# Kernel tuning notes

Hardware: AMD Instinct MI355X
Metric: run time of the kernel (lower is better)

Reference implementation:

```python
import jax, jax.numpy as jnp
import numpy as np

C = 512
IC = C // 2
BN_EPS = 1e-5

def conv1x1(x, w, b):
    # x: (b,c,h,w), w: (o,c), b: (o,)
    return jnp.einsum('bchw,oc->bohw', x, w) + b[None, :, None, None]

def setup_inputs() -> dict:
    key = jax.random.key(0)
    ks = jax.random.split(key, 9)
    b, h, w = 8, 48, 48
    x = jax.random.normal(ks[0], (b, C, h, w), dtype=jnp.float32)
    s = 1.0 / np.sqrt(C)
    g_w = jax.random.normal(ks[1], (IC, C), dtype=jnp.float32) * s
    g_b = jnp.zeros((IC,), jnp.float32)
    theta_w = jax.random.normal(ks[2], (IC, C), dtype=jnp.float32) * s
    theta_b = jnp.zeros((IC,), jnp.float32)
    phi_w = jax.random.normal(ks[3], (IC, C), dtype=jnp.float32) * s
    phi_b = jnp.zeros((IC,), jnp.float32)
    w_w = jax.random.normal(ks[4], (C, IC), dtype=jnp.float32) * (1.0 / np.sqrt(IC))
    w_b = jnp.zeros((C,), jnp.float32)
    # BatchNorm affine params: initialized to 0 per nn.init.constant_ in source
    bn_gamma = jnp.zeros((C,), jnp.float32)
    bn_beta = jnp.zeros((C,), jnp.float32)
    return {"x": x, "g_w": g_w, "g_b": g_b, "theta_w": theta_w, "theta_b": theta_b,
            "phi_w": phi_w, "phi_b": phi_b, "w_w": w_w, "w_b": w_b,
            "bn_gamma": bn_gamma, "bn_beta": bn_beta}

def reference(x, g_w, g_b, theta_w, theta_b, phi_w, phi_b, w_w, w_b, bn_gamma, bn_beta):
    b, c, h, w = x.shape
    hw = h * w
    g_x = conv1x1(x, g_w, g_b).reshape(b, IC, hw).transpose(0, 2, 1)      # (b,hw,ic)
    theta_x = conv1x1(x, theta_w, theta_b).reshape(b, IC, hw).transpose(0, 2, 1)  # (b,hw,ic)
    phi_x = conv1x1(x, phi_w, phi_b).reshape(b, IC, hw)                    # (b,ic,hw)
    f = jnp.einsum('bqc,bck->bqk', theta_x, phi_x)                         # (b,hw,hw), unscaled
    f_div_C = jax.nn.softmax(f, axis=-1)
    y = jnp.einsum('bqk,bkc->bqc', f_div_C, g_x)                           # (b,hw,ic)
    y = y.transpose(0, 2, 1).reshape(b, IC, h, w)
    wy = conv1x1(y, w_w, w_b)                                              # (b,c,h,w)
    # BatchNorm2d in training mode: batch statistics over (b,h,w)
    mean = jnp.mean(wy, axis=(0, 2, 3), keepdims=True)
    var = jnp.var(wy, axis=(0, 2, 3), keepdims=True)
    wy_bn = (wy - mean) / jnp.sqrt(var + BN_EPS)
    wy_bn = wy_bn * bn_gamma[None, :, None, None] + bn_beta[None, :, None, None]
    return wy_bn + x
```

## Files before the change

### kernel.cpp

```cpp
#include <hip/hip_runtime.h>
#include <hip/hip_bf16.h>
#include <stdint.h>

constexpr int Bn  = 8;
constexpr int Cc  = 512;
constexpr int ICc = 256;
constexpr int HWc = 48 * 48;
constexpr float BN_EPS = 1e-5f;

typedef unsigned short u16;
typedef __attribute__((ext_vector_type(8))) short short8;
typedef __attribute__((ext_vector_type(4))) float f32x4;

__device__ __forceinline__ u16 f2bf(float f) {
    uint32_t u = __builtin_bit_cast(uint32_t, f);
    u += 0x7fffu + ((u >> 16) & 1u);
    return (u16)(u >> 16);
}
__device__ __forceinline__ float bf2f(u16 h) {
    uint32_t u = ((uint32_t)h) << 16;
    return __builtin_bit_cast(float, u);
}
__device__ __forceinline__ void load_lds16(const void* g, void* l) {
    __builtin_amdgcn_global_load_lds(
        (const __attribute__((address_space(1))) void*)(uintptr_t)g,
        (__attribute__((address_space(3))) void*)(uintptr_t)l, 16, 0, 0);
}
template <int N> __device__ __forceinline__ void wait_vmcnt() {
    if constexpr (N == 0)      asm volatile("s_waitcnt vmcnt(0)" ::: "memory");
    else if constexpr (N == 3) asm volatile("s_waitcnt vmcnt(3)" ::: "memory");
    else if constexpr (N == 4) asm volatile("s_waitcnt vmcnt(4)" ::: "memory");
    else if constexpr (N == 6) asm volatile("s_waitcnt vmcnt(6)" ::: "memory");
    else if constexpr (N == 8) asm volatile("s_waitcnt vmcnt(8)" ::: "memory");
}
__device__ __forceinline__ void wait_lgkm0() {
    asm volatile("s_waitcnt lgkmcnt(0)" ::: "memory");
}
__device__ __forceinline__ void barrier_fenced() {
    __builtin_amdgcn_s_barrier();
    asm volatile("" ::: "memory");
}

__global__ __launch_bounds__(256)
void cast_front(const float* __restrict__ th_w, const float* __restrict__ ph_w,
                const float* __restrict__ g_w, const float* __restrict__ th_b,
                const float* __restrict__ ph_b, u16* __restrict__ wcat,
                float* __restrict__ bias_thph) {
    int idx = blockIdx.x * 256 + threadIdx.x;
    if (idx < 98304) {
        const float4* src;
        if (idx < 32768)       src = (const float4*)th_w + idx;
        else if (idx < 65536)  src = (const float4*)ph_w + (idx - 32768);
        else                   src = (const float4*)g_w  + (idx - 65536);
        float4 v = *src;
        ushort4 o;
        o.x = f2bf(v.x); o.y = f2bf(v.y); o.z = f2bf(v.z); o.w = f2bf(v.w);
        ((ushort4*)wcat)[idx] = o;
    } else if (idx < 98816) {
        int i = idx - 98304;
        bias_thph[i] = (i < 256) ? th_b[i] : ph_b[i - 256];
    }
}

__global__ __launch_bounds__(256)
void cast_w(const float* __restrict__ a, u16* __restrict__ out) {
    int idx = blockIdx.x * 256 + threadIdx.x;
    float4 v = ((const float4*)a)[idx];
    ushort4 o;
    o.x = f2bf(v.x); o.y = f2bf(v.y); o.z = f2bf(v.z); o.w = f2bf(v.w);
    ((ushort4*)out)[idx] = o;
}

__global__ __launch_bounds__(256)
void transpose_cast_x(const float* __restrict__ x, u16* __restrict__ xt) {
    __shared__ float t[64][33];
    const int b = blockIdx.z;
    const int p0 = blockIdx.x * 32;
    const int c0 = blockIdx.y * 64;
    const int tx = threadIdx.x & 31, ty = threadIdx.x >> 5;
    const float* xb = x + (size_t)b * Cc * HWc;
#pragma unroll
    for (int r = 0; r < 8; ++r)
        t[r * 8 + ty][tx] = xb[(size_t)(c0 + r * 8 + ty) * HWc + p0 + tx];
    __syncthreads();
    u16* xtb = xt + (size_t)b * HWc * Cc;
    const int cc = (threadIdx.x & 31) * 2, pp = threadIdx.x >> 5;
#pragma unroll
    for (int r = 0; r < 4; ++r) {
        int p = r * 8 + pp;
        ushort2 v;
        v.x = f2bf(t[cc][p]);
        v.y = f2bf(t[cc + 1][p]);
        *(ushort2*)&xtb[(size_t)(p0 + p) * Cc + c0 + cc] = v;
    }
}

template <int TM, int STORE, bool STATS>
__global__ __launch_bounds__(256, 2)
void mfma_gemm(const u16* __restrict__ A, const u16* __restrict__ B,
               void* __restrict__ Cout, const float* __restrict__ bias,
               int bias_mode, int K, int ldA, int ldB, int ldC,
               size_t sA, size_t sB, size_t sC,
               float* __restrict__ s0g, float* __restrict__ s1g) {
    constexpr int MI  = TM / 32;
    constexpr int LPS = (TM == 128) ? 4 : 3;
    __shared__ __align__(16) u16 As[3][TM * 32];
    __shared__ __align__(16) u16 Bs[3][128 * 32];
    const int bz = blockIdx.z;
    const int m0 = blockIdx.y * TM, n0 = blockIdx.x * 128;
    const u16* Ab = A + (size_t)bz * sA + (size_t)m0 * ldA;
    const u16* Bb = B + (size_t)bz * sB + (size_t)n0 * ldB;
    const int tid = threadIdx.x, lane = tid & 63, w = tid >> 6;
    const int wm = (w & 1) * (TM / 2);
    const int wn = (w >> 1) * 64;
    const int quad = lane >> 4, m16 = lane & 15;

    f32x4 acc[MI][4];
#pragma unroll
    for (int i = 0; i < MI; ++i)
#pragma unroll
        for (int j = 0; j < 4; ++j) acc[i][j] = (f32x4){0.f, 0.f, 0.f, 0.f};

    const int L0 = 2 * w * 64 + lane, L1 = L0 + 64;
    const int br0 = L0 >> 2, bc0 = ((L0 & 3) ^ ((L0 >> 3) & 3)) * 8;
    const int br1 = L1 >> 2, bc1 = ((L1 & 3) ^ ((L1 >> 3) & 3)) * 8;
    const int ar0 = (TM == 128) ? br0 : (tid >> 2);
    const int ac0 = (TM == 128) ? bc0 : (((tid & 3) ^ ((tid >> 3) & 3)) * 8);

    auto stage = [&](int buf, int k0) {
        if (TM == 128) {
            load_lds16(Ab + (size_t)ar0 * ldA + k0 + ac0, &As[buf][2 * w * 512]);
            load_lds16(Ab + (size_t)br1 * ldA + k0 + bc1, &As[buf][(2 * w + 1) * 512]);
        } else {
            load_lds16(Ab + (size_t)ar0 * ldA + k0 + ac0, &As[buf][w * 512]);
        }
        load_lds16(Bb + (size_t)br0 * ldB + k0 + bc0, &Bs[buf][2 * w * 512]);
        load_lds16(Bb + (size_t)br1 * ldB + k0 + bc1, &Bs[buf][(2 * w + 1) * 512]);
    };

    const int sq = (quad ^ ((m16 >> 1) & 3)) * 8;

    auto compute = [&](int buf) {
        short8 af[MI], bfv[4];
#pragma unroll
        for (int i = 0; i < MI; ++i)
            af[i] = *(const short8*)&As[buf][(wm + i * 16 + m16) * 32 + sq];
#pragma unroll
        for (int j = 0; j < 4; ++j)
            bfv[j] = *(const short8*)&Bs[buf][(wn + j * 16 + m16) * 32 + sq];
#pragma unroll
        for (int i = 0; i < MI; ++i)
#pragma unroll
            for (int j = 0; j < 4; ++j)
                acc[i][j] = __builtin_amdgcn_mfma_f32_16x16x32_bf16(
                    af[i], bfv[j], acc[i][j], 0, 0, 0);
    };

    const int nt = K / 32;
    stage(0, 0);
    stage(1, 32);

    int cur = 0;
    for (int t = 0; t < nt - 2; ++t) {
        int nxt = cur + 2; if (nxt >= 3) nxt -= 3;
        stage(nxt, (t + 2) * 32);
        wait_vmcnt<2 * LPS>();
        barrier_fenced();
        compute(cur);
        wait_lgkm0();
        barrier_fenced();
        ++cur; if (cur == 3) cur = 0;
    }
    wait_vmcnt<LPS>();
    barrier_fenced();
    compute(cur);
    wait_lgkm0();
    barrier_fenced();
    ++cur; if (cur == 3) cur = 0;
    wait_vmcnt<0>();
    barrier_fenced();
    compute(cur);

    if (bias_mode) {
#pragma unroll
        for (int i = 0; i < MI; ++i)
#pragma unroll
            for (int j = 0; j < 4; ++j)
#pragma unroll
                for (int r = 0; r < 4; ++r)
                    acc[i][j][r] += (bias_mode == 2)
                        ? bias[m0 + wm + i * 16 + quad * 4 + r]
                        : bias[n0 + wn + j * 16 + m16];
    }

    if (STORE == 0) {
        u16* C = (u16*)Cout + (size_t)bz * sC;
#pragma unroll
        for (int i = 0; i < MI; ++i) {
            int m = m0 + wm + i * 16 + quad * 4;
#pragma unroll
            for (int j = 0; j < 4; ++j) {
                int n = n0 + wn + j * 16 + m16;
#pragma unroll
                for (int r = 0; r < 4; ++r)
                    C[(size_t)(m + r) * ldC + n] = f2bf(acc[i][j][r]);
            }
        }
    } else {
        float* C = (float*)Cout + (size_t)bz * sC;
#pragma unroll
        for (int i = 0; i < MI; ++i) {
            int m = m0 + wm + i * 16 + quad * 4;
#pragma unroll
            for (int j = 0; j < 4; ++j) {
                int n = n0 + wn + j * 16 + m16;
#pragma unroll
                for (int r = 0; r < 4; ++r)
                    C[(size_t)(m + r) * ldC + n] = acc[i][j][r];
            }
        }
    }

    if (STATS) {
#pragma unroll
        for (int i = 0; i < MI; ++i) {
#pragma unroll
            for (int r = 0; r < 4; ++r) {
                float v0 = 0.f, v1 = 0.f;
#pragma unroll
                for (int j = 0; j < 4; ++j) {
                    float v = acc[i][j][r];
                    v0 += v;
                    v1 = fmaf(v, v, v1);
                }
#pragma unroll
                for (int off = 8; off; off >>= 1) {
                    v0 += __shfl_down(v0, off, 16);
                    v1 += __shfl_down(v1, off, 16);
                }
                if (m16 == 0) {
                    int m = m0 + wm + i * 16 + quad * 4 + r;
                    atomicAdd(&s0g[m], v0);
                    atomicAdd(&s1g[m], v1);
                }
            }
        }
    }
}

__global__ __launch_bounds__(256, 2)
void fused_attn(const u16* __restrict__ thph, const u16* __restrict__ gmat,
                u16* __restrict__ y) {
    __shared__ __align__(16) u16 Ks[2][64 * 256];
    __shared__ __align__(16) u16 Sl[64 * 68];
    __shared__ float alpha_lds[64];

    const int id = blockIdx.x;
    const int b = id & 7, qi = id >> 3;
    const int q0 = qi * 64;
    const u16* tB = thph + (size_t)b * HWc * 512;
    const u16* gB = gmat + (size_t)b * ICc * HWc;
    const int tid = threadIdx.x, lane = tid & 63, w = tid >> 6;
    const int quad = lane >> 4, m16 = lane & 15;
    const int wq = (w & 1) * 32, wk = (w >> 1) * 32;
    const int wv = w * 64;

    short8 qf[2][8];
#pragma unroll
    for (int i = 0; i < 2; ++i)
#pragma unroll
        for (int ds = 0; ds < 8; ++ds)
            qf[i][ds] = *(const short8*)&tB[(size_t)(q0 + wq + i * 16 + m16) * 512
                                            + ds * 32 + quad * 8];

    auto stageK = [&](int buf, int k0) {
#pragma unroll
        for (int u = 0; u < 8; ++u) {
            int s = (w * 8 + u) * 64 + lane;
            int r = s >> 5;
            int c = s & 31;
            int sc = c ^ (r & 7);
            load_lds16(tB + (size_t)(k0 + r) * 512 + 256 + sc * 8,
                       &Ks[buf][(w * 8 + u) * 512]);
        }
    };

    const int sr = w * 16 + (lane >> 2);
    const int scol = (lane & 3) * 16;
    float mrow = -3.0e38f, lrow = 0.f;

    f32x4 acc2[4][4];
#pragma unroll
    for (int i = 0; i < 4; ++i)
#pragma unroll
        for (int j = 0; j < 4; ++j) acc2[i][j] = (f32x4){0.f, 0.f, 0.f, 0.f};

    stageK(0, 0);

    for (int t = 0; t < 36; ++t) {
        const int buf = t & 1;
        if (t + 1 < 36) {
            stageK(buf ^ 1, (t + 1) * 64);
            wait_vmcnt<8>();
        } else {
            wait_vmcnt<0>();
        }
        barrier_fenced();

        f32x4 acc1[2][2];
#pragma unroll
        for (int i = 0; i < 2; ++i)
#pragma unroll
            for (int j = 0; j < 2; ++j) acc1[i][j] = (f32x4){0.f, 0.f, 0.f, 0.f};
        const u16* kb = &Ks[buf][0];
#pragma unroll
        for (int ds = 0; ds < 8; ++ds) {
            short8 kf[2];
#pragma unroll
            for (int j = 0; j < 2; ++j) {
                int kr = wk + j * 16 + m16;
                int c  = (ds * 4 + quad) ^ (m16 & 7);
                kf[j] = *(const short8*)&kb[kr * 256 + c * 8];
            }
#pragma unroll
            for (int i = 0; i < 2; ++i)
#pragma unroll
                for (int j = 0; j < 2; ++j)
                    acc1[i][j] = __builtin_amdgcn_mfma_f32_16x16x32_bf16(
                        qf[i][ds], kf[j], acc1[i][j], 0, 0, 0);
        }

#pragma unroll
        for (int i = 0; i < 2; ++i)
#pragma unroll
            for (int j = 0; j < 2; ++j)
#pragma unroll
                for (int r = 0; r < 4; ++r)
                    Sl[(wq + i * 16 + quad * 4 + r) * 68 + wk + j * 16 + m16] =
                        f2bf(acc1[i][j][r]);
        wait_lgkm0();
        barrier_fenced();

        {
            u16* srow = &Sl[sr * 68 + scol];
            float v[16];
            short4 r0 = *(const short4*)&srow[0];
            short4 r1 = *(const short4*)&srow[4];
            short4 r2 = *(const short4*)&srow[8];
            short4 r3 = *(const short4*)&srow[12];
            v[0]=bf2f((u16)r0.x); v[1]=bf2f((u16)r0.y); v[2]=bf2f((u16)r0.z); v[3]=bf2f((u16)r0.w);
            v[4]=bf2f((u16)r1.x); v[5]=bf2f((u16)r1.y); v[6]=bf2f((u16)r1.z); v[7]=bf2f((u16)r1.w);
            v[8]=bf2f((u16)r2.x); v[9]=bf2f((u16)r2.y); v[10]=bf2f((u16)r2.z); v[11]=bf2f((u16)r2.w);
            v[12]=bf2f((u16)r3.x); v[13]=bf2f((u16)r3.y); v[14]=bf2f((u16)r3.z); v[15]=bf2f((u16)r3.w);
            float tm = v[0];
#pragma unroll
            for (int k = 1; k < 16; ++k) tm = fmaxf(tm, v[k]);
            tm = fmaxf(tm, __shfl_xor(tm, 1, 64));
            tm = fmaxf(tm, __shfl_xor(tm, 2, 64));
            float mn = fmaxf(mrow, tm);
            float a  = __expf(mrow - mn);
            float rs = 0.f;
#pragma unroll
            for (int k = 0; k < 16; ++k) { v[k] = __expf(v[k] - mn); rs += v[k]; }
            rs += __shfl_xor(rs, 1, 64);
            rs += __shfl_xor(rs, 2, 64);
            lrow = lrow * a + rs;
            mrow = mn;
            ushort4 o0 = {f2bf(v[0]), f2bf(v[1]), f2bf(v[2]), f2bf(v[3])};
            ushort4 o1 = {f2bf(v[4]), f2bf(v[5]), f2bf(v[6]), f2bf(v[7])};
            ushort4 o2 = {f2bf(v[8]), f2bf(v[9]), f2bf(v[10]), f2bf(v[11])};
            ushort4 o3 = {f2bf(v[12]), f2bf(v[13]), f2bf(v[14]), f2bf(v[15])};
            *(ushort4*)&srow[0]  = o0;
            *(ushort4*)&srow[4]  = o1;
            *(ushort4*)&srow[8]  = o2;
            *(ushort4*)&srow[12] = o3;
            if ((lane & 3) == 0) alpha_lds[sr] = a;
        }
        wait_lgkm0();
        barrier_fenced();

        f32x4 al[4];
#pragma unroll
        for (int i = 0; i < 4; ++i)
            al[i] = *(const f32x4*)&alpha_lds[i * 16 + quad * 4];
#pragma unroll
        for (int i = 0; i < 4; ++i)
#pragma unroll
            for (int j2 = 0; j2 < 4; ++j2)
#pragma unroll
                for (int r = 0; r < 4; ++r) acc2[i][j2][r] *= al[i][r];

        const int kbase = t * 64;
#pragma unroll
        for (int ks = 0; ks < 2; ++ks) {
            short8 pa[4];
#pragma unroll
            for (int i = 0; i < 4; ++i) {
                const u16* pr = &Sl[(i * 16 + m16) * 68 + ks * 32 + quad * 8];
                short4 lo = *(const short4*)&pr[0];
                short4 hi = *(const short4*)&pr[4];
                pa[i] = (short8){lo.x, lo.y, lo.z, lo.w, hi.x, hi.y, hi.z, hi.w};
            }
            short8 vb[4];
#pragma unroll
            for (int j2 = 0; j2 < 4; ++j2)
                vb[j2] = *(const short8*)&gB[(size_t)(wv + j2 * 16 + m16) * HWc
                                             + kbase + ks * 32 + quad * 8];
#pragma unroll
            for (int i = 0; i < 4; ++i)
#pragma unroll
                for (int j2 = 0; j2 < 4; ++j2)
                    acc2[i][j2] = __builtin_amdgcn_mfma_f32_16x16x32_bf16(
                        pa[i], vb[j2], acc2[i][j2], 0, 0, 0);
        }
    }

    __syncthreads();
    if ((lane & 3) == 0) alpha_lds[sr] = 1.0f / lrow;
    __syncthreads();

    u16* yB = y + (size_t)b * HWc * ICc;
#pragma unroll
    for (int i = 0; i < 4; ++i) {
        f32x4 li = *(const f32x4*)&alpha_lds[i * 16 + quad * 4];
#pragma unroll
        for (int j2 = 0; j2 < 4; ++j2)
#pragma unroll
            for (int r = 0; r < 4; ++r)
                yB[(size_t)(q0 + i * 16 + quad * 4 + r) * ICc + wv + j2 * 16 + m16] =
                    f2bf(acc2[i][j2][r] * li[r]);
    }
}

__global__ __launch_bounds__(256)
void bn_apply(const float* __restrict__ wy, const float* __restrict__ x,
              const float* __restrict__ s0, const float* __restrict__ s1,
              const float* __restrict__ gamma, const float* __restrict__ beta,
              float* __restrict__ out) {
    const size_t i4 = (size_t)blockIdx.x * 256 + threadIdx.x;
    const size_t base = i4 * 4;
    const int o = (int)((base / HWc) % Cc);
    const float N = (float)(Bn * HWc);
    const float mean = s0[o] / N;
    const float var  = s1[o] / N - mean * mean;
    const float rstd = rsqrtf(var + BN_EPS);
    const float ga = gamma[o];
    const float be = beta[o];
    const float4 w4 = ((const float4*)wy)[i4];
    const float4 x4 = ((const float4*)x)[i4];
    float4 r;
    r.x = (w4.x - mean) * rstd * ga + be + x4.x;
    r.y = (w4.y - mean) * rstd * ga + be + x4.y;
    r.z = (w4.z - mean) * rstd * ga + be + x4.z;
    r.w = (w4.w - mean) * rstd * ga + be + x4.w;
    ((float4*)out)[i4] = r;
}

extern "C" void kernel_launch(void* const* d_in, const int* in_sizes, int n_in,
                              void* d_out, int out_size, void* d_ws, size_t ws_size,
                              hipStream_t stream) {
    const float* x     = (const float*)d_in[0];
    const float* g_w   = (const float*)d_in[1];
    const float* g_b   = (const float*)d_in[2];
    const float* th_w  = (const float*)d_in[3];
    const float* th_b  = (const float*)d_in[4];
    const float* ph_w  = (const float*)d_in[5];
    const float* ph_b  = (const float*)d_in[6];
    const float* w_w   = (const float*)d_in[7];
    const float* w_b   = (const float*)d_in[8];
    const float* gamma = (const float*)d_in[9];
    const float* beta  = (const float*)d_in[10];

    char* base = (char*)d_ws;
    const size_t SZT = (size_t)Bn * HWc * ICc * 2;
    u16* thph = (u16*)base;
    u16* g    = (u16*)(base + 2 * SZT);
    char* Sreg = base + 3 * SZT;
    u16* xt   = (u16*)Sreg;
    u16* wcat = (u16*)(Sreg + (size_t)Bn * HWc * Cc * 2);
    float* bias_thph = (float*)(Sreg + (size_t)Bn * HWc * Cc * 2 + 786432);
    u16* y    = (u16*)Sreg;
    float* wy = (float*)(Sreg + SZT);
    u16* wbf2 = (u16*)(Sreg + SZT + (size_t)Bn * Cc * HWc * 4);
    float* stats = (float*)(Sreg + SZT + (size_t)Bn * Cc * HWc * 4 + 262144);

    dim3 blk(256);
    const u16* thphw = wcat;
    const u16* gwb   = wcat + 262144;

    cast_front<<<dim3(386), blk, 0, stream>>>(th_w, ph_w, g_w, th_b, ph_b,
                                              wcat, bias_thph);
    transpose_cast_x<<<dim3(HWc / 32, Cc / 64, Bn), blk, 0, stream>>>(x, xt);

    mfma_gemm<128, 0, false><<<dim3(4, 18, Bn), blk, 0, stream>>>(
        xt, thphw, thph, bias_thph, 1, Cc, Cc, Cc, 512,
        (size_t)HWc * Cc, 0, (size_t)HWc * 512, nullptr, nullptr);

    mfma_gemm<64, 0, false><<<dim3(18, 4, Bn), blk, 0, stream>>>(
        gwb, xt, g, g_b, 2, Cc, Cc, Cc, HWc,
        0, (size_t)HWc * Cc, (size_t)ICc * HWc, nullptr, nullptr);

    cast_w<<<dim3(128), blk, 0, stream>>>(w_w, wbf2);
    hipMemsetAsync(stats, 0, 2 * Cc * sizeof(float), stream);

    fused_attn<<<dim3(288), blk, 0, stream>>>(thph, g, y);

    mfma_gemm<128, 1, true><<<dim3(18, 4, Bn), blk, 0, stream>>>(
        wbf2, y, wy, w_b, 2, ICc, ICc, ICc, HWc,
        0, (size_t)HWc * ICc, (size_t)Cc * HWc, stats, stats + Cc);

    bn_apply<<<dim3((Bn * Cc * HWc) / 4 / 256), blk, 0, stream>>>(
        wy, x, stats, stats + Cc, gamma, beta, (float*)d_out);
}
```

Before: 323.1 us.

## Halve attention query and key tiles to double blocks and occupancy

New measurement: 394.9 us. 1.22x slower.

```diff
diff --git a/kernel.cpp b/kernel.cpp
--- a/kernel.cpp
+++ b/kernel.cpp
@@ -248,180 +248,149 @@
     }
 }
 
-__global__ __launch_bounds__(256, 2)
+__global__ __launch_bounds__(256, 4)
 void fused_attn(const u16* __restrict__ thph, const u16* __restrict__ gmat,
                 u16* __restrict__ y) {
-    __shared__ __align__(16) u16 Ks[2][64 * 256];
-    __shared__ __align__(16) u16 Sl[64 * 68];
-    __shared__ float alpha_lds[64];
+    __shared__ __align__(16) u16 Ks[2][32 * 256];
+    __shared__ __align__(16) u16 Sl[32 * 36];
+    __shared__ __align__(16) float alpha_lds[32];
 
     const int id = blockIdx.x;
     const int b = id & 7, qi = id >> 3;
-    const int q0 = qi * 64;
+    const int q0 = qi * 32;
     const u16* tB = thph + (size_t)b * HWc * 512;
     const u16* gB = gmat + (size_t)b * ICc * HWc;
     const int tid = threadIdx.x, lane = tid & 63, w = tid >> 6;
     const int quad = lane >> 4, m16 = lane & 15;
-    const int wq = (w & 1) * 32, wk = (w >> 1) * 32;
+    const int wq = (w & 1) * 16, wk = (w >> 1) * 16;
     const int wv = w * 64;
 
-    short8 qf[2][8];
-#pragma unroll
-    for (int i = 0; i < 2; ++i)
-#pragma unroll
-        for (int ds = 0; ds < 8; ++ds)
-            qf[i][ds] = *(const short8*)&tB[(size_t)(q0 + wq + i * 16 + m16) * 512
-                                            + ds * 32 + quad * 8];
+    short8 qf[8];
+#pragma unroll
+    for (int ds = 0; ds < 8; ++ds)
+        qf[ds] = *(const short8*)&tB[(size_t)(q0 + wq + m16) * 512
+                                     + ds * 32 + quad * 8];
 
     auto stageK = [&](int buf, int k0) {
 #pragma unroll
-        for (int u = 0; u < 8; ++u) {
-            int s = (w * 8 + u) * 64 + lane;
+        for (int u = 0; u < 4; ++u) {
+            int s = (w * 4 + u) * 64 + lane;
             int r = s >> 5;
             int c = s & 31;
             int sc = c ^ (r & 7);
             load_lds16(tB + (size_t)(k0 + r) * 512 + 256 + sc * 8,
-                       &Ks[buf][(w * 8 + u) * 512]);
+                       &Ks[buf][(w * 4 + u) * 512]);
         }
     };
 
-    const int sr = w * 16 + (lane >> 2);
-    const int scol = (lane & 3) * 16;
+    const int sr = tid >> 3;
+    const int sc0 = (tid & 7) * 4;
     float mrow = -3.0e38f, lrow = 0.f;
 
-    f32x4 acc2[4][4];
-#pragma unroll
-    for (int i = 0; i < 4; ++i)
+    f32x4 acc2[2][4];
+#pragma unroll
+    for (int i = 0; i < 2; ++i)
 #pragma unroll
         for (int j = 0; j < 4; ++j) acc2[i][j] = (f32x4){0.f, 0.f, 0.f, 0.f};
 
     stageK(0, 0);
-
-    for (int t = 0; t < 36; ++t) {
+    wait_vmcnt<0>();
+
+    for (int t = 0; t < 72; ++t) {
         const int buf = t & 1;
-        if (t + 1 < 36) {
-            stageK(buf ^ 1, (t + 1) * 64);
+        const int kbase = t * 32;
+
+        short8 vb[4];
+#pragma unroll
+        for (int j2 = 0; j2 < 4; ++j2)
+            vb[j2] = *(const short8*)&gB[(size_t)(wv + j2 * 16 + m16) * HWc
+                                         + kbase + quad * 8];
+        if (t + 1 < 72) {
+            stageK(buf ^ 1, (t + 1) * 32);
             wait_vmcnt<8>();
         } else {
-            wait_vmcnt<0>();
+            wait_vmcnt<4>();
         }
         barrier_fenced();
 
-        f32x4 acc1[2][2];
-#pragma unroll
-        for (int i = 0; i < 2; ++i)
-#pragma unroll
-            for (int j = 0; j < 2; ++j) acc1[i][j] = (f32x4){0.f, 0.f, 0.f, 0.f};
-        const u16* kb = &Ks[buf][0];
-#pragma unroll
-        for (int ds = 0; ds < 8; ++ds) {
-            short8 kf[2];
-#pragma unroll
-            for (int j = 0; j < 2; ++j) {
-                int kr = wk + j * 16 + m16;
-                int c  = (ds * 4 + quad) ^ (m16 & 7);
-                kf[j] = *(const short8*)&kb[kr * 256 + c * 8];
+        f32x4 acc1 = (f32x4){0.f, 0.f, 0.f, 0.f};
+        {
+            const u16* kb = &Ks[buf][0];
+            const int krow = (wk + m16) * 256;
+            const int kx = m16 & 7;
+#pragma unroll
+            for (int ds = 0; ds < 8; ++ds) {
+                short8 kf = *(const short8*)&kb[krow + ((ds * 4 + quad) ^ kx) * 8];
+                acc1 = __builtin_amdgcn_mfma_f32_16x16x32_bf16(
+                    qf[ds], kf, acc1, 0, 0, 0);
             }
-#pragma unroll
-            for (int i = 0; i < 2; ++i)
-#pragma unroll
-                for (int j = 0; j < 2; ++j)
-                    acc1[i][j] = __builtin_amdgcn_mfma_f32_16x16x32_bf16(
-                        qf[i][ds], kf[j], acc1[i][j], 0, 0, 0);
-        }
-
-#pragma unroll
-        for (int i = 0; i < 2; ++i)
-#pragma unroll
-            for (int j = 0; j < 2; ++j)
-#pragma unroll
-                for (int r = 0; r < 4; ++r)
-                    Sl[(wq + i * 16 + quad * 4 + r) * 68 + wk + j * 16 + m16] =
-                        f2bf(acc1[i][j][r]);
+        }
+#pragma unroll
+        for (int r = 0; r < 4; ++r)
+            Sl[(wq + quad * 4 + r) * 36 + wk + m16] = f2bf(acc1[r]);
         wait_lgkm0();
         barrier_fenced();
 
         {
-            u16* srow = &Sl[sr * 68 + scol];
-            float v[16];
-            short4 r0 = *(const short4*)&srow[0];
-            short4 r1 = *(const short4*)&srow[4];
-            short4 r2 = *(const short4*)&srow[8];
-            short4 r3 = *(const short4*)&srow[12];
-            v[0]=bf2f((u16)r0.x); v[1]=bf2f((u16)r0.y); v[2]=bf2f((u16)r0.z); v[3]=bf2f((u16)r0.w);
-            v[4]=bf2f((u16)r1.x); v[5]=bf2f((u16)r1.y); v[6]=bf2f((u16)r1.z); v[7]=bf2f((u16)r1.w);
-            v[8]=bf2f((u16)r2.x); v[9]=bf2f((u16)r2.y); v[10]=bf2f((u16)r2.z); v[11]=bf2f((u16)r2.w);
-            v[12]=bf2f((u16)r3.x); v[13]=bf2f((u16)r3.y); v[14]=bf2f((u16)r3.z); v[15]=bf2f((u16)r3.w);
-            float tm = v[0];
-#pragma unroll
-            for (int k = 1; k < 16; ++k) tm = fmaxf(tm, v[k]);
+            u16* srow = &Sl[sr * 36 + sc0];
+            ushort4 raw = *(const ushort4*)srow;
+            float v0 = bf2f(raw.x), v1 = bf2f(raw.y);
+            float v2 = bf2f(raw.z), v3 = bf2f(raw.w);
+            float tm = fmaxf(fmaxf(v0, v1), fmaxf(v2, v3));
             tm = fmaxf(tm, __shfl_xor(tm, 1, 64));
             tm = fmaxf(tm, __shfl_xor(tm, 2, 64));
+            tm = fmaxf(tm, __shfl_xor(tm, 4, 64));
             float mn = fmaxf(mrow, tm);
             float a  = __expf(mrow - mn);
-            float rs = 0.f;
-#pragma unroll
-            for (int k = 0; k < 16; ++k) { v[k] = __expf(v[k] - mn); rs += v[k]; }
+            v0 = __expf(v0 - mn); v1 = __expf(v1 - mn);
+            v2 = __expf(v2 - mn); v3 = __expf(v3 - mn);
+            float rs = (v0 + v1) + (v2 + v3);
             rs += __shfl_xor(rs, 1, 64);
             rs += __shfl_xor(rs, 2, 64);
+            rs += __shfl_xor(rs, 4, 64);
             lrow = lrow * a + rs;
             mrow = mn;
-            ushort4 o0 = {f2bf(v[0]), f2bf(v[1]), f2bf(v[2]), f2bf(v[3])};
-            ushort4 o1 = {f2bf(v[4]), f2bf(v[5]), f2bf(v[6]), f2bf(v[7])};
-            ushort4 o2 = {f2bf(v[8]), f2bf(v[9]), f2bf(v[10]), f2bf(v[11])};
-            ushort4 o3 = {f2bf(v[12]), f2bf(v[13]), f2bf(v[14]), f2bf(v[15])};
-            *(ushort4*)&srow[0]  = o0;
-            *(ushort4*)&srow[4]  = o1;
-            *(ushort4*)&srow[8]  = o2;
-            *(ushort4*)&srow[12] = o3;
-            if ((lane & 3) == 0) alpha_lds[sr] = a;
+            ushort4 o = {f2bf(v0), f2bf(v1), f2bf(v2), f2bf(v3)};
+            *(ushort4*)srow = o;
+            if ((tid & 7) == 0) alpha_lds[sr] = a;
         }
         wait_lgkm0();
         barrier_fenced();
 
-        f32x4 al[4];
-#pragma unroll
-        for (int i = 0; i < 4; ++i)
-            al[i] = *(const f32x4*)&alpha_lds[i * 16 + quad * 4];
-#pragma unroll
-        for (int i = 0; i < 4; ++i)
+#pragma unroll
+        for (int i = 0; i < 2; ++i) {
+            f32x4 al = *(const f32x4*)&alpha_lds[i * 16 + quad * 4];
 #pragma unroll
             for (int j2 = 0; j2 < 4; ++j2)
 #pragma unroll
-                for (int r = 0; r < 4; ++r) acc2[i][j2][r] *= al[i][r];
-
-        const int kbase = t * 64;
-#pragma unroll
-        for (int ks = 0; ks < 2; ++ks) {
-            short8 pa[4];
-#pragma unroll
-            for (int i = 0; i < 4; ++i) {
-                const u16* pr = &Sl[(i * 16 + m16) * 68 + ks * 32 + quad * 8];
-                short4 lo = *(const short4*)&pr[0];
-                short4 hi = *(const short4*)&pr[4];
-                pa[i] = (short8){lo.x, lo.y, lo.z, lo.w, hi.x, hi.y, hi.z, hi.w};
-            }
-            short8 vb[4];
+                for (int r = 0; r < 4; ++r) acc2[i][j2][r] *= al[r];
+        }
+
+        if (t + 1 < 72) wait_vmcnt<4>();
+        else            wait_vmcnt<0>();
+        short8 pa[2];
+#pragma unroll
+        for (int i = 0; i < 2; ++i) {
+            const u16* pr = &Sl[(i * 16 + m16) * 36 + quad * 8];
+            short4 lo = *(const short4*)&pr[0];
+            short4 hi = *(const short4*)&pr[4];
+            pa[i] = (short8){lo.x, lo.y, lo.z, lo.w, hi.x, hi.y, hi.z, hi.w};
+        }
+#pragma unroll
+        for (int i = 0; i < 2; ++i)
 #pragma unroll
             for (int j2 = 0; j2 < 4; ++j2)
-                vb[j2] = *(const short8*)&gB[(size_t)(wv + j2 * 16 + m16) * HWc
-                                             + kbase + ks * 32 + quad * 8];
-#pragma unroll
-            for (int i = 0; i < 4; ++i)
-#pragma unroll
-                for (int j2 = 0; j2 < 4; ++j2)
-                    acc2[i][j2] = __builtin_amdgcn_mfma_f32_16x16x32_bf16(
-                        pa[i], vb[j2], acc2[i][j2], 0, 0, 0);
-        }
+                acc2[i][j2] = __builtin_amdgcn_mfma_f32_16x16x32_bf16(
+                    pa[i], vb[j2], acc2[i][j2], 0, 0, 0);
     }
 
     __syncthreads();
-    if ((lane & 3) == 0) alpha_lds[sr] = 1.0f / lrow;
+    if ((tid & 7) == 0) alpha_lds[sr] = 1.0f / lrow;
     __syncthreads();
 
     u16* yB = y + (size_t)b * HWc * ICc;
 #pragma unroll
-    for (int i = 0; i < 4; ++i) {
+    for (int i = 0; i < 2; ++i) {
         f32x4 li = *(const f32x4*)&alpha_lds[i * 16 + quad * 4];
 #pragma unroll
         for (int j2 = 0; j2 < 4; ++j2)
@@ -503,7 +472,7 @@
     cast_w<<<dim3(128), blk, 0, stream>>>(w_w, wbf2);
     hipMemsetAsync(stats, 0, 2 * Cc * sizeof(float), stream);
 
-    fused_attn<<<dim3(288), blk, 0, stream>>>(thph, g, y);
+    fused_attn<<<dim3(576), blk, 0, stream>>>(thph, g, y);
 
     mfma_gemm<128, 1, true><<<dim3(18, 4, Bn), blk, 0, stream>>>(
         wbf2, y, wy, w_b, 2, ICc, ICc, ICc, HWc,
```

## Split attention over key halves and keep softmax in registers

Applied to the files above, without the earlier changes.

New measurement: 361.5 us. 11.9% more time.

```diff
diff --git a/kernel.cpp b/kernel.cpp
--- a/kernel.cpp
+++ b/kernel.cpp
@@ -250,186 +250,198 @@
 
 __global__ __launch_bounds__(256, 2)
 void fused_attn(const u16* __restrict__ thph, const u16* __restrict__ gmat,
-                u16* __restrict__ y) {
+                float* __restrict__ Np, float* __restrict__ Ml) {
     __shared__ __align__(16) u16 Ks[2][64 * 256];
-    __shared__ __align__(16) u16 Sl[64 * 68];
-    __shared__ float alpha_lds[64];
+    __shared__ __align__(16) u16 Sl[64 * 64];
+    __shared__ __align__(16) float alpha_lds[64];
 
     const int id = blockIdx.x;
-    const int b = id & 7, qi = id >> 3;
+    const int b  = id & 7;
+    const int s  = (id >> 3) & 1;
+    const int qi = id >> 4;
     const int q0 = qi * 64;
+    const int kofs = s * 1152;
     const u16* tB = thph + (size_t)b * HWc * 512;
     const u16* gB = gmat + (size_t)b * ICc * HWc;
     const int tid = threadIdx.x, lane = tid & 63, w = tid >> 6;
     const int quad = lane >> 4, m16 = lane & 15;
-    const int wq = (w & 1) * 32, wk = (w >> 1) * 32;
+    const int wq = w * 16;
     const int wv = w * 64;
-
-    short8 qf[2][8];
-#pragma unroll
-    for (int i = 0; i < 2; ++i)
-#pragma unroll
-        for (int ds = 0; ds < 8; ++ds)
-            qf[i][ds] = *(const short8*)&tB[(size_t)(q0 + wq + i * 16 + m16) * 512
-                                            + ds * 32 + quad * 8];
-
-    auto stageK = [&](int buf, int k0) {
+    const int kx = m16 & 7;
+
+    short8 qf[8];
+#pragma unroll
+    for (int ds = 0; ds < 8; ++ds)
+        qf[ds] = *(const short8*)&tB[(size_t)(q0 + wq + m16) * 512
+                                     + ds * 32 + quad * 8];
+
+    auto stageK = [&](int buf, int t) {
+        const int k0 = kofs + t * 64;
 #pragma unroll
         for (int u = 0; u < 8; ++u) {
-            int s = (w * 8 + u) * 64 + lane;
-            int r = s >> 5;
-            int c = s & 31;
-            int sc = c ^ (r & 7);
-            load_lds16(tB + (size_t)(k0 + r) * 512 + 256 + sc * 8,
+            int sidx = (w * 8 + u) * 64 + lane;
+            int r = sidx >> 5;
+            int c = sidx & 31;
+            load_lds16(tB + (size_t)(k0 + r) * 512 + 256 + (c ^ (r & 7)) * 8,
                        &Ks[buf][(w * 8 + u) * 512]);
         }
     };
 
-    const int sr = w * 16 + (lane >> 2);
-    const int scol = (lane & 3) * 16;
-    float mrow = -3.0e38f, lrow = 0.f;
-
+    f32x4 mrow = (f32x4){-3.0e38f, -3.0e38f, -3.0e38f, -3.0e38f};
+    f32x4 lrow = (f32x4){0.f, 0.f, 0.f, 0.f};
     f32x4 acc2[4][4];
 #pragma unroll
     for (int i = 0; i < 4; ++i)
 #pragma unroll
         for (int j = 0; j < 4; ++j) acc2[i][j] = (f32x4){0.f, 0.f, 0.f, 0.f};
 
+    short8 vb[4][2];
+    auto loadV = [&](int t) {
+        const int kb = kofs + t * 64;
+#pragma unroll
+        for (int j2 = 0; j2 < 4; ++j2)
+#pragma unroll
+            for (int ks = 0; ks < 2; ++ks)
+                vb[j2][ks] = *(const short8*)&gB[(size_t)(wv + j2 * 16 + m16) * HWc
+                                                 + kb + ks * 32 + quad * 8];
+    };
+
     stageK(0, 0);
-
-    for (int t = 0; t < 36; ++t) {
+    loadV(0);
+    wait_vmcnt<0>();
+    barrier_fenced();
+
+    constexpr int NT = 18;
+    for (int t = 0; t < NT; ++t) {
         const int buf = t & 1;
-        if (t + 1 < 36) {
-            stageK(buf ^ 1, (t + 1) * 64);
-            wait_vmcnt<8>();
-        } else {
-            wait_vmcnt<0>();
-        }
-        barrier_fenced();
-
-        f32x4 acc1[2][2];
-#pragma unroll
-        for (int i = 0; i < 2; ++i)
-#pragma unroll
-            for (int j = 0; j < 2; ++j) acc1[i][j] = (f32x4){0.f, 0.f, 0.f, 0.f};
-        const u16* kb = &Ks[buf][0];
-#pragma unroll
-        for (int ds = 0; ds < 8; ++ds) {
-            short8 kf[2];
-#pragma unroll
-            for (int j = 0; j < 2; ++j) {
-                int kr = wk + j * 16 + m16;
-                int c  = (ds * 4 + quad) ^ (m16 & 7);
-                kf[j] = *(const short8*)&kb[kr * 256 + c * 8];
+
+        f32x4 acc1[4];
+#pragma unroll
+        for (int kf = 0; kf < 4; ++kf) acc1[kf] = (f32x4){0.f, 0.f, 0.f, 0.f};
+        {
+            const u16* kb = &Ks[buf][0];
+#pragma unroll
+            for (int ds = 0; ds < 8; ++ds) {
+#pragma unroll
+                for (int kf = 0; kf < 4; ++kf) {
+                    short8 kfr = *(const short8*)
+                        &kb[(kf * 16 + m16) * 256 + (((ds * 4 + quad) ^ kx) * 8)];
+                    acc1[kf] = __builtin_amdgcn_mfma_f32_16x16x32_bf16(
+                        qf[ds], kfr, acc1[kf], 0, 0, 0);
+                }
             }
-#pragma unroll
-            for (int i = 0; i < 2; ++i)
-#pragma unroll
-                for (int j = 0; j < 2; ++j)
-                    acc1[i][j] = __builtin_amdgcn_mfma_f32_16x16x32_bf16(
-                        qf[i][ds], kf[j], acc1[i][j], 0, 0, 0);
-        }
-
-#pragma unroll
-        for (int i = 0; i < 2; ++i)
-#pragma unroll
-            for (int j = 0; j < 2; ++j)
-#pragma unroll
-                for (int r = 0; r < 4; ++r)
-                    Sl[(wq + i * 16 + quad * 4 + r) * 68 + wk + j * 16 + m16] =
-                        f2bf(acc1[i][j][r]);
+        }
+        if (t + 1 < NT) stageK(buf ^ 1, t + 1);
+
+        f32x4 aalpha;
+#pragma unroll
+        for (int r = 0; r < 4; ++r) {
+            float tm = fmaxf(fmaxf(acc1[0][r], acc1[1][r]),
+                             fmaxf(acc1[2][r], acc1[3][r]));
+            tm = fmaxf(tm, __shfl_xor(tm, 1, 64));
+            tm = fmaxf(tm, __shfl_xor(tm, 2, 64));
+            tm = fmaxf(tm, __shfl_xor(tm, 4, 64));
+            tm = fmaxf(tm, __shfl_xor(tm, 8, 64));
+            float mn = fmaxf(mrow[r], tm);
+            aalpha[r] = __expf(mrow[r] - mn);
+            float rs = 0.f;
+#pragma unroll
+            for (int kf = 0; kf < 4; ++kf) {
+                float p = __expf(acc1[kf][r] - mn);
+                acc1[kf][r] = p;
+                rs += p;
+            }
+            rs += __shfl_xor(rs, 1, 64);
+            rs += __shfl_xor(rs, 2, 64);
+            rs += __shfl_xor(rs, 4, 64);
+            rs += __shfl_xor(rs, 8, 64);
+            lrow[r] = lrow[r] * aalpha[r] + rs;
+            mrow[r] = mn;
+        }
+#pragma unroll
+        for (int kf = 0; kf < 4; ++kf)
+#pragma unroll
+            for (int r = 0; r < 4; ++r) {
+                int row = wq + quad * 4 + r;
+                int col = (kf * 16 + m16) ^ (((quad * 4 + r) & 7) << 3);
+                Sl[row * 64 + col] = f2bf(acc1[kf][r]);
+            }
+        if (m16 == 0) {
+#pragma unroll
+            for (int r = 0; r < 4; ++r)
+                alpha_lds[wq + quad * 4 + r] = aalpha[r];
+        }
         wait_lgkm0();
         barrier_fenced();
 
-        {
-            u16* srow = &Sl[sr * 68 + scol];
-            float v[16];
-            short4 r0 = *(const short4*)&srow[0];
-            short4 r1 = *(const short4*)&srow[4];
-            short4 r2 = *(const short4*)&srow[8];
-            short4 r3 = *(const short4*)&srow[12];
-            v[0]=bf2f((u16)r0.x); v[1]=bf2f((u16)r0.y); v[2]=bf2f((u16)r0.z); v[3]=bf2f((u16)r0.w);
-            v[4]=bf2f((u16)r1.x); v[5]=bf2f((u16)r1.y); v[6]=bf2f((u16)r1.z); v[7]=bf2f((u16)r1.w);
-            v[8]=bf2f((u16)r2.x); v[9]=bf2f((u16)r2.y); v[10]=bf2f((u16)r2.z); v[11]=bf2f((u16)r2.w);
-            v[12]=bf2f((u16)r3.x); v[13]=bf2f((u16)r3.y); v[14]=bf2f((u16)r3.z); v[15]=bf2f((u16)r3.w);
-            float tm = v[0];
-#pragma unroll
-            for (int k = 1; k < 16; ++k) tm = fmaxf(tm, v[k]);
-            tm = fmaxf(tm, __shfl_xor(tm, 1, 64));
-            tm = fmaxf(tm, __shfl_xor(tm, 2, 64));
-            float mn = fmaxf(mrow, tm);
-            float a  = __expf(mrow - mn);
-            float rs = 0.f;
-#pragma unroll
-            for (int k = 0; k < 16; ++k) { v[k] = __expf(v[k] - mn); rs += v[k]; }
-            rs += __shfl_xor(rs, 1, 64);
-            rs += __shfl_xor(rs, 2, 64);
-            lrow = lrow * a + rs;
-            mrow = mn;
-            ushort4 o0 = {f2bf(v[0]), f2bf(v[1]), f2bf(v[2]), f2bf(v[3])};
-            ushort4 o1 = {f2bf(v[4]), f2bf(v[5]), f2bf(v[6]), f2bf(v[7])};
-            ushort4 o2 = {f2bf(v[8]), f2bf(v[9]), f2bf(v[10]), f2bf(v[11])};
-            ushort4 o3 = {f2bf(v[12]), f2bf(v[13]), f2bf(v[14]), f2bf(v[15])};
-            *(ushort4*)&srow[0]  = o0;
-            *(ushort4*)&srow[4]  = o1;
-            *(ushort4*)&srow[8]  = o2;
-            *(ushort4*)&srow[12] = o3;
-            if ((lane & 3) == 0) alpha_lds[sr] = a;
-        }
-        wait_lgkm0();
-        barrier_fenced();
-
-        f32x4 al[4];
-#pragma unroll
-        for (int i = 0; i < 4; ++i)
-            al[i] = *(const f32x4*)&alpha_lds[i * 16 + quad * 4];
-#pragma unroll
-        for (int i = 0; i < 4; ++i)
+#pragma unroll
+        for (int i = 0; i < 4; ++i) {
+            f32x4 al = *(const f32x4*)&alpha_lds[i * 16 + quad * 4];
 #pragma unroll
             for (int j2 = 0; j2 < 4; ++j2)
 #pragma unroll
-                for (int r = 0; r < 4; ++r) acc2[i][j2][r] *= al[i][r];
-
-        const int kbase = t * 64;
+                for (int r = 0; r < 4; ++r) acc2[i][j2][r] *= al[r];
+        }
+
 #pragma unroll
         for (int ks = 0; ks < 2; ++ks) {
             short8 pa[4];
 #pragma unroll
-            for (int i = 0; i < 4; ++i) {
-                const u16* pr = &Sl[(i * 16 + m16) * 68 + ks * 32 + quad * 8];
-                short4 lo = *(const short4*)&pr[0];
-                short4 hi = *(const short4*)&pr[4];
-                pa[i] = (short8){lo.x, lo.y, lo.z, lo.w, hi.x, hi.y, hi.z, hi.w};
-            }
-            short8 vb[4];
-#pragma unroll
-            for (int j2 = 0; j2 < 4; ++j2)
-                vb[j2] = *(const short8*)&gB[(size_t)(wv + j2 * 16 + m16) * HWc
-                                             + kbase + ks * 32 + quad * 8];
+            for (int i = 0; i < 4; ++i)
+                pa[i] = *(const short8*)
+                    &Sl[(i * 16 + m16) * 64 + (((ks * 4 + quad) ^ kx) * 8)];
 #pragma unroll
             for (int i = 0; i < 4; ++i)
 #pragma unroll
                 for (int j2 = 0; j2 < 4; ++j2)
                     acc2[i][j2] = __builtin_amdgcn_mfma_f32_16x16x32_bf16(
-                        pa[i], vb[j2], acc2[i][j2], 0, 0, 0);
-        }
-    }
-
-    __syncthreads();
-    if ((lane & 3) == 0) alpha_lds[sr] = 1.0f / lrow;
-    __syncthreads();
-
-    u16* yB = y + (size_t)b * HWc * ICc;
-#pragma unroll
-    for (int i = 0; i < 4; ++i) {
-        f32x4 li = *(const f32x4*)&alpha_lds[i * 16 + quad * 4];
+                        pa[i], vb[j2][ks], acc2[i][j2], 0, 0, 0);
+        }
+
+        if (t + 1 < NT) {
+            loadV(t + 1);
+            wait_vmcnt<8>();
+        }
+        barrier_fenced();
+    }
+
+    float* NpB = Np + ((size_t)s * 8 + b) * ((size_t)HWc * ICc);
+#pragma unroll
+    for (int i = 0; i < 4; ++i)
 #pragma unroll
         for (int j2 = 0; j2 < 4; ++j2)
 #pragma unroll
             for (int r = 0; r < 4; ++r)
-                yB[(size_t)(q0 + i * 16 + quad * 4 + r) * ICc + wv + j2 * 16 + m16] =
-                    f2bf(acc2[i][j2][r] * li[r]);
-    }
+                NpB[(size_t)(q0 + i * 16 + quad * 4 + r) * ICc
+                    + wv + j2 * 16 + m16] = acc2[i][j2][r];
+    if (m16 == 0) {
+#pragma unroll
+        for (int r = 0; r < 4; ++r) {
+            int row = q0 + wq + quad * 4 + r;
+            Ml[(size_t)(s * 2 + 0) * (8 * HWc) + b * HWc + row] = mrow[r];
+            Ml[(size_t)(s * 2 + 1) * (8 * HWc) + b * HWc + row] = lrow[r];
+        }
+    }
+}
+
+__global__ __launch_bounds__(256)
+void combine_y(const float* __restrict__ Np, const float* __restrict__ Ml,
+               u16* __restrict__ y) {
+    const size_t i4 = (size_t)blockIdx.x * 256 + threadIdx.x;
+    const int bq = (int)((i4 * 4) >> 8);
+    const float m0 = Ml[bq],                l0 = Ml[8 * HWc + bq];
+    const float m1 = Ml[2 * 8 * HWc + bq],  l1 = Ml[3 * 8 * HWc + bq];
+    const float M  = fmaxf(m0, m1);
+    const float e0 = __expf(m0 - M), e1 = __expf(m1 - M);
+    const float inv = 1.0f / (l0 * e0 + l1 * e1);
+    const float4 n0 = ((const float4*)Np)[i4];
+    const float4 n1 = ((const float4*)(Np + (size_t)8 * HWc * ICc))[i4];
+    ushort4 o;
+    o.x = f2bf((n0.x * e0 + n1.x * e1) * inv);
+    o.y = f2bf((n0.y * e0 + n1.y * e1) * inv);
+    o.z = f2bf((n0.z * e0 + n1.z * e1) * inv);
+    o.w = f2bf((n0.w * e0 + n1.w * e1) * inv);
+    ((ushort4*)y)[i4] = o;
 }
 
 __global__ __launch_bounds__(256)
@@ -479,10 +491,12 @@
     u16* xt   = (u16*)Sreg;
     u16* wcat = (u16*)(Sreg + (size_t)Bn * HWc * Cc * 2);
     float* bias_thph = (float*)(Sreg + (size_t)Bn * HWc * Cc * 2 + 786432);
-    u16* y    = (u16*)Sreg;
-    float* wy = (float*)(Sreg + SZT);
-    u16* wbf2 = (u16*)(Sreg + SZT + (size_t)Bn * Cc * HWc * 4);
-    float* stats = (float*)(Sreg + SZT + (size_t)Bn * Cc * HWc * 4 + 262144);
+    float* Np = (float*)Sreg;
+    float* Ml = (float*)(Sreg + 40u * 1024 * 1024);
+    u16* wbf2 = (u16*)(Sreg + 42u * 1024 * 1024);
+    float* stats = (float*)(Sreg + 43u * 1024 * 1024);
+    u16* y    = (u16*)base;
+    float* wy = (float*)Sreg;
 
     dim3 blk(256);
     const u16* thphw = wcat;
@@ -503,7 +517,9 @@
     cast_w<<<dim3(128), blk, 0, stream>>>(w_w, wbf2);
     hipMemsetAsync(stats, 0, 2 * Cc * sizeof(float), stream);
 
-    fused_attn<<<dim3(288), blk, 0, stream>>>(thph, g, y);
+    fused_attn<<<dim3(576), blk, 0, stream>>>(thph, g, Np, Ml);
+
+    combine_y<<<dim3((8 * HWc * ICc / 4) / 256), blk, 0, stream>>>(Np, Ml, y);
 
     mfma_gemm<128, 1, true><<<dim3(18, 4, Bn), blk, 0, stream>>>(
         wbf2, y, wy, w_b, 2, ICc, ICc, ICc, HWc,
```
